# Optimization experiments

Hardware: AMD Instinct MI355X
Metric: run time of the kernel (lower is better)

Reference implementation:

```python
import jax, jax.numpy as jnp
import numpy as np

B, C, H, W = 64, 3, 512, 512
MIN = 0.33  # min crop fraction from __init__


def setup_inputs() -> dict:
    key = jax.random.key(0)
    k1, k2, k3, k4, k5 = jax.random.split(key, 5)
    img = jax.random.normal(k1, (B, C, H, W), jnp.float32)
    # Replicate the module's internal randint sampling for the crop boxes.
    min_h, min_w = int(MIN * H), int(MIN * W)
    hight = jax.random.randint(k2, (B,), min_h, H)
    width = jax.random.randint(k3, (B,), min_w, W)
    yc = jax.random.randint(k4, (B,), min_h // 2, H)
    xc = jax.random.randint(k5, (B,), min_w // 2, W)
    y1 = jnp.clip(yc - hight // 2, 0, H).astype(jnp.int32)
    y2 = jnp.clip(yc + hight // 2, 0, H).astype(jnp.int32)
    x1 = jnp.clip(xc - width // 2, 0, W).astype(jnp.int32)
    x2 = jnp.clip(xc + width // 2, 0, W).astype(jnp.int32)
    return {"img": img, "y1": y1, "y2": y2, "x1": x1, "x2": x2}


def _axis_coords(start, end, out_size):
    # Source coords for bilinear resize, align_corners=False (torch default).
    n = (end - start).astype(jnp.float32)  # crop length along this axis
    s = (jnp.arange(out_size, dtype=jnp.float32) + 0.5) * n / out_size - 0.5
    s = jnp.clip(s, 0.0, n - 1.0)
    i0 = jnp.floor(s).astype(jnp.int32)
    i1 = jnp.minimum(i0 + 1, end - start - 1)
    wgt = s - i0.astype(jnp.float32)
    return start + i0, start + i1, wgt  # absolute indices into the full image


def _resize_one(img_b, y1, y2, x1, x2):
    # img_b: [C, H, W]; crop [y1:y2, x1:x2] then bilinear-resize back to (H, W)
    iy0, iy1, wy = _axis_coords(y1, y2, H)
    ix0, ix1, wx = _axis_coords(x1, x2, W)
    r0 = jnp.take(img_b, iy0, axis=1)
    r1 = jnp.take(img_b, iy1, axis=1)
    rows = r0 + (r1 - r0) * wy[None, :, None]      # [C, H, W] rows interpolated
    c0 = jnp.take(rows, ix0, axis=2)
    c1 = jnp.take(rows, ix1, axis=2)
    return c0 + (c1 - c0) * wx[None, None, :]      # [C, H, W]


def reference(img, y1, y2, x1, x2):
    return jax.vmap(_resize_one)(img, y1, y2, x1, x2)
```

## Files before the change

### kernel.cpp

```cpp
#include <hip/hip_runtime.h>


#define BB 64
#define CC 3
#define HH 512
#define WW 512
#define NB (BB * HH)
#define PITCH 516

__global__ __launch_bounds__(256) void rand_crop_resize_kernel(
    const float* __restrict__ img,
    const int* __restrict__ y1a, const int* __restrict__ y2a,
    const int* __restrict__ x1a, const int* __restrict__ x2a,
    float* __restrict__ out)
{
    __shared__ float s[6 * PITCH];

    const int r  = (blockIdx.x & 7) * (NB / 8) + (blockIdx.x >> 3);
    const int oy = r & (HH - 1);
    const int b  = r >> 9;

    const int Y1 = y1a[b], Y2 = y2a[b], X1 = x1a[b], X2 = x2a[b];

    const int ny_i = Y2 - Y1;
    float sy = ((float)oy + 0.5f) * (float)ny_i * (1.0f / 512.0f) - 0.5f;
    sy = fminf(fmaxf(sy, 0.0f), (float)ny_i - 1.0f);
    int iy0 = (int)sy;
    const int iy1 = min(iy0 + 1, ny_i - 1) + Y1;
    const float wy = sy - (float)iy0;
    iy0 += Y1;

    const int t = threadIdx.x;

    const int nx_i = X2 - X1;
    const int c0   = X1 >> 2;
    const int c1   = min((X1 + nx_i) >> 2, (WW >> 2) - 1);
    const int nch  = c1 - c0 + 1;
    const int xoff = X1 - (c0 << 2);
    const int zi   = xoff + nx_i;

    if (t < 6) s[t * PITCH + zi] = 0.0f;

    const size_t base = (size_t)b * (size_t)(CC * HH * WW);
    const int g  = t >> 7;
    const int tt = t & 127;
    if (tt < nch) {
        #pragma unroll
        for (int k = 0; k < 3; ++k) {
            const int rw = g * 3 + k;
            const int c  = rw >> 1;
            const int iy = (rw & 1) ? iy1 : iy0;
            const float4 v = ((const float4*)(img + base
                                 + (size_t)(c * HH + iy) * (size_t)WW))[c0 + tt];
            ((float4*)(s + rw * PITCH))[tt] = v;
        }
    }
    __syncthreads();

    const float nx    = (float)nx_i;
    const float nxm1f = nx - 1.0f;

    float2 res[3];
    #pragma unroll
    for (int k = 0; k < 2; ++k) {
        const int ox = 2 * t + k;
        float sx = ((float)ox + 0.5f) * nx * (1.0f / 512.0f) - 0.5f;
        sx = fminf(fmaxf(sx, 0.0f), nxm1f);
        const int   ix0 = (int)sx;
        const float wx  = sx - (float)ix0;
        const int   ix  = xoff + ix0;

        #pragma unroll
        for (int c = 0; c < 3; ++c) {
            const float* s0 = s + (2 * c) * PITCH;
            const float* s1 = s0 + PITCH;
            const float v00 = s0[ix];
            const float v01 = s0[ix + 1];
            const float v10 = s1[ix];
            const float v11 = s1[ix + 1];
            const float r0 = v00 + (v10 - v00) * wy;
            const float r1 = v01 + (v11 - v01) * wy;
            const float v  = r0 + (r1 - r0) * wx;
            if (k == 0) res[c].x = v; else res[c].y = v;
        }
    }

    #pragma unroll
    for (int c = 0; c < 3; ++c) {
        float2* orow = (float2*)(out
            + ((size_t)(b * CC + c) * (size_t)HH + (size_t)oy) * (size_t)WW);
        orow[t] = res[c];
    }
}

extern "C" void kernel_launch(void* const* d_in, const int* in_sizes, int n_in,
                              void* d_out, int out_size, void* d_ws, size_t ws_size,
                              hipStream_t stream) {
    const float* img = (const float*)d_in[0];
    const int*   y1  = (const int*)d_in[1];
    const int*   y2  = (const int*)d_in[2];
    const int*   x1  = (const int*)d_in[3];
    const int*   x2  = (const int*)d_in[4];
    float*       out = (float*)d_out;

    dim3 grid(NB);
    dim3 block(256);
    hipLaunchKernelGGL(rand_crop_resize_kernel, grid, block, 0, stream,
                       img, y1, y2, x1, x2, out);
}
```

Measured before the change: 320.8 us.

## Process eight output rows per block with register double-buffered row prefetch

Each block now handles eight consecutive output rows instead of one, and the grid shrinks by eight. The per-column x coordinates and weights are computed once and reused across rows. Source rows for the next output row are loaded into registers while the current row is interpolated from LDS, which overlaps global loads with compute and amortizes block setup. The cost is fewer blocks (4096) and more barriers per block, which may lower occupancy-driven latency hiding. Adjacent rows often reuse the same source rows, but they are reloaded anyway.

```diff
diff --git a/kernel.cpp b/kernel.cpp
--- a/kernel.cpp
+++ b/kernel.cpp
@@ -6,7 +6,12 @@
 #define HH 512
 #define WW 512
 #define NB (BB * HH)
+#define TILES 8
+#define NBLK (NB / TILES)
 #define PITCH 516
+
+#define BAR() do { asm volatile("s_waitcnt lgkmcnt(0)" ::: "memory"); \
+                   __builtin_amdgcn_s_barrier(); } while (0)
 
 __global__ __launch_bounds__(256) void rand_crop_resize_kernel(
     const float* __restrict__ img,
@@ -16,21 +21,18 @@
 {
     __shared__ float s[6 * PITCH];
 
-    const int r  = (blockIdx.x & 7) * (NB / 8) + (blockIdx.x >> 3);
-    const int oy = r & (HH - 1);
-    const int b  = r >> 9;
+    const int j   = (blockIdx.x & 7) * (NBLK / 8) + (blockIdx.x >> 3);
+    const int r0  = j * TILES;
+    const int b   = r0 >> 9;
+    const int oy0 = r0 & (HH - 1);
 
     const int Y1 = y1a[b], Y2 = y2a[b], X1 = x1a[b], X2 = x2a[b];
+    const int   ny_i = Y2 - Y1;
+    const float nyf  = (float)ny_i;
 
-    const int ny_i = Y2 - Y1;
-    float sy = ((float)oy + 0.5f) * (float)ny_i * (1.0f / 512.0f) - 0.5f;
-    sy = fminf(fmaxf(sy, 0.0f), (float)ny_i - 1.0f);
-    int iy0 = (int)sy;
-    const int iy1 = min(iy0 + 1, ny_i - 1) + Y1;
-    const float wy = sy - (float)iy0;
-    iy0 += Y1;
-
-    const int t = threadIdx.x;
+    const int t  = threadIdx.x;
+    const int g  = t >> 7;
+    const int tt = t & 127;
 
     const int nx_i = X2 - X1;
     const int c0   = X1 >> 2;
@@ -41,55 +43,101 @@
 
     if (t < 6) s[t * PITCH + zi] = 0.0f;
 
-    const size_t base = (size_t)b * (size_t)(CC * HH * WW);
-    const int g  = t >> 7;
-    const int tt = t & 127;
-    if (tt < nch) {
-        #pragma unroll
-        for (int k = 0; k < 3; ++k) {
-            const int rw = g * 3 + k;
-            const int c  = rw >> 1;
-            const int iy = (rw & 1) ? iy1 : iy0;
-            const float4 v = ((const float4*)(img + base
-                                 + (size_t)(c * HH + iy) * (size_t)WW))[c0 + tt];
-            ((float4*)(s + rw * PITCH))[tt] = v;
-        }
-    }
-    __syncthreads();
-
-    const float nx    = (float)nx_i;
-    const float nxm1f = nx - 1.0f;
-
-    float2 res[3];
+    const float nx = (float)nx_i, nxm1f = nx - 1.0f;
+    int ixk[2]; float wxk[2];
     #pragma unroll
     for (int k = 0; k < 2; ++k) {
         const int ox = 2 * t + k;
         float sx = ((float)ox + 0.5f) * nx * (1.0f / 512.0f) - 0.5f;
         sx = fminf(fmaxf(sx, 0.0f), nxm1f);
-        const int   ix0 = (int)sx;
-        const float wx  = sx - (float)ix0;
-        const int   ix  = xoff + ix0;
+        const int ix0 = (int)sx;
+        wxk[k] = sx - (float)ix0;
+        ixk[k] = xoff + ix0;
+    }
 
+    const size_t base = (size_t)b * (size_t)(CC * HH * WW);
+
+    auto ycoord = [&](int oy, int& iy0, int& iy1, float& wy) {
+        float sy = ((float)oy + 0.5f) * nyf * (1.0f / 512.0f) - 0.5f;
+        sy = fminf(fmaxf(sy, 0.0f), nyf - 1.0f);
+        const int i0 = (int)sy;
+        wy  = sy - (float)i0;
+        iy1 = min(i0 + 1, ny_i - 1) + Y1;
+        iy0 = i0 + Y1;
+    };
+
+    auto issue = [&](int iy0t, int iy1t, float4* buf) {
+        if (tt < nch) {
+            #pragma unroll
+            for (int k = 0; k < 3; ++k) {
+                const int rw = 3 * g + k;
+                const int c  = rw >> 1;
+                const int iy = (rw & 1) ? iy1t : iy0t;
+                buf[k] = ((const float4*)(img + base
+                             + (size_t)(c * HH + iy) * (size_t)WW))[c0 + tt];
+            }
+        }
+    };
+
+    auto commit = [&](const float4* buf) {
+        if (tt < nch) {
+            #pragma unroll
+            for (int k = 0; k < 3; ++k)
+                ((float4*)(s + (3 * g + k) * PITCH))[tt] = buf[k];
+        }
+    };
+
+    auto gather = [&](int oy, float wy) {
+        float2 res[3];
+        #pragma unroll
+        for (int k = 0; k < 2; ++k) {
+            const int   ix = ixk[k];
+            const float wx = wxk[k];
+            #pragma unroll
+            for (int c = 0; c < 3; ++c) {
+                const float* s0 = s + (2 * c) * PITCH;
+                const float* s1 = s0 + PITCH;
+                const float v00 = s0[ix];
+                const float v01 = s0[ix + 1];
+                const float v10 = s1[ix];
+                const float v11 = s1[ix + 1];
+                const float r0v = v00 + (v10 - v00) * wy;
+                const float r1v = v01 + (v11 - v01) * wy;
+                const float v   = r0v + (r1v - r0v) * wx;
+                if (k == 0) res[c].x = v; else res[c].y = v;
+            }
+        }
         #pragma unroll
         for (int c = 0; c < 3; ++c) {
-            const float* s0 = s + (2 * c) * PITCH;
-            const float* s1 = s0 + PITCH;
-            const float v00 = s0[ix];
-            const float v01 = s0[ix + 1];
-            const float v10 = s1[ix];
-            const float v11 = s1[ix + 1];
-            const float r0 = v00 + (v10 - v00) * wy;
-            const float r1 = v01 + (v11 - v01) * wy;
-            const float v  = r0 + (r1 - r0) * wx;
-            if (k == 0) res[c].x = v; else res[c].y = v;
+            float2* orow = (float2*)(out
+                + ((size_t)(b * CC + c) * (size_t)HH + (size_t)oy) * (size_t)WW);
+            orow[t] = res[c];
         }
-    }
+    };
+
+    float4 A[3] = {}, B[3] = {};
+    int iy0t, iy1t; float wyA, wyB;
+
+    ycoord(oy0, iy0t, iy1t, wyA);
+    issue(iy0t, iy1t, A);
 
     #pragma unroll
-    for (int c = 0; c < 3; ++c) {
-        float2* orow = (float2*)(out
-            + ((size_t)(b * CC + c) * (size_t)HH + (size_t)oy) * (size_t)WW);
-        orow[t] = res[c];
+    for (int itp = 0; itp < TILES; itp += 2) {
+        commit(A);
+        ycoord(oy0 + itp + 1, iy0t, iy1t, wyB);
+        issue(iy0t, iy1t, B);
+        BAR();
+        gather(oy0 + itp, wyA);
+        BAR();
+
+        commit(B);
+        if (itp + 2 < TILES) {
+            ycoord(oy0 + itp + 2, iy0t, iy1t, wyA);
+            issue(iy0t, iy1t, A);
+        }
+        BAR();
+        gather(oy0 + itp + 1, wyB);
+        BAR();
     }
 }
 
@@ -103,7 +151,7 @@
     const int*   x2  = (const int*)d_in[4];
     float*       out = (float*)d_out;
 
-    dim3 grid(NB);
+    dim3 grid(NBLK);
     dim3 block(256);
     hipLaunchKernelGGL(rand_crop_resize_kernel, grid, block, 0, stream,
                        img, y1, y2, x1, x2, out);
```

New measurement: 441.4 us. +37.6%, slower.
